# Optimization experiments

Measured on AMD Instinct MI355X. Metric: run time of the kernel, lower is better.

Reference implementation:

```python
import jax, jax.numpy as jnp
import numpy as np

H = 64  # hidden_size


def lstm_layer(x, Wih, Whh, bih, bhh):
    """Single LSTM layer, batch_first input x: [B, T, D]. Returns (hs [B,T,H], h_last [B,H]).
    PyTorch gate order: i, f, g, o."""
    B, T, _ = x.shape
    # Precompute input projections for all timesteps: [T, B, 4H]
    xg = jnp.einsum('btd,gd->tbg', x, Wih) + (bih + bhh)

    def step(carry, xt):
        h, c = carry
        gates = xt + h @ Whh.T  # [B, 4H]
        i, f, g, o = jnp.split(gates, 4, axis=-1)
        i = jax.nn.sigmoid(i)
        f = jax.nn.sigmoid(f)
        g = jnp.tanh(g)
        o = jax.nn.sigmoid(o)
        c = f * c + i * g
        h = o * jnp.tanh(c)
        return (h, c), h

    h0 = jnp.zeros((B, H), dtype=x.dtype)
    c0 = jnp.zeros((B, H), dtype=x.dtype)
    (h_last, _), hs = jax.lax.scan(step, (h0, c0), xg)
    return jnp.transpose(hs, (1, 0, 2)), h_last  # [B,T,H], [B,H]


def setup_inputs() -> dict:
    key = jax.random.key(0)
    ks = jax.random.split(key, 11)
    B, T, D = 1024, 512, 6
    s0 = 1.0 / np.sqrt(H)
    u = lambda k, shp: jax.random.uniform(k, shp, jnp.float32, -s0, s0)
    return {
        'x': jax.random.normal(ks[0], (B, T, D), jnp.float32),
        'Wih0': u(ks[1], (4 * H, D)),
        'Whh0': u(ks[2], (4 * H, H)),
        'bih0': u(ks[3], (4 * H,)),
        'bhh0': u(ks[4], (4 * H,)),
        'Wih1': u(ks[5], (4 * H, H)),
        'Whh1': u(ks[6], (4 * H, H)),
        'bih1': u(ks[7], (4 * H,)),
        'bhh1': u(ks[8], (4 * H,)),
        'W1': u(ks[9], (32, H)),
        'b1': jnp.zeros((32,), jnp.float32),
        'W2': u(ks[10], (1, 32)),
        'b2': jnp.zeros((1,), jnp.float32),
    }


def reference(x, Wih0, Whh0, bih0, bhh0, Wih1, Whh1, bih1, bhh1, W1, b1, W2, b2):
    # Layer 0 (dropout between layers is identity in eval mode)
    hs0, _ = lstm_layer(x, Wih0, Whh0, bih0, bhh0)
    # Layer 1: only last hidden state needed
    _, h_last = lstm_layer(hs0, Wih1, Whh1, bih1, bhh1)
    # MLP head: Linear -> ReLU -> (Dropout=identity) -> Linear -> Sigmoid
    z = jax.nn.relu(h_last @ W1.T + b1)
    out = jax.nn.sigmoid(z @ W2.T + b2)
    return out.squeeze()  # [B]
```

## Files before the change

kernel.cpp:

```cpp
#include <hip/hip_runtime.h>
#include <cstdint>

#define Hh 64
#define Tt 512
#define Dd 6
#define BB 4
#define NT 512
#define XS_STRIDE 3080
#define PREW 512

typedef short bf16x8 __attribute__((ext_vector_type(8)));
typedef float f32x4  __attribute__((ext_vector_type(4)));

#define MF(A, B, C) C = __builtin_amdgcn_mfma_f32_16x16x32_bf16(A, B, C, 0, 0, 0)

__device__ __forceinline__ float sigm(float v){
  return __builtin_amdgcn_rcpf(1.f + __expf(-v));
}
__device__ __forceinline__ float tanh_(float v){
  return 1.f - 2.f*__builtin_amdgcn_rcpf(1.f + __expf(2.f*v));
}
__device__ __forceinline__ unsigned short f2bf(float f){
  union { float f; unsigned u; } v; v.f = f;
  unsigned r = v.u + 0x7FFFu + ((v.u >> 16) & 1u);
  return (unsigned short)(r >> 16);
}
__device__ __forceinline__ float bf2f(unsigned short b){
  union { unsigned u; float f; } v; v.u = ((unsigned)b) << 16;
  return v.f;
}
__device__ __forceinline__ void split8(const float* w, bf16x8& hi, bf16x8& lo){
  #pragma unroll
  for (int i = 0; i < 8; ++i){
    unsigned short h_ = f2bf(w[i]);
    hi[i] = (short)h_;
    lo[i] = (short)f2bf(w[i] - bf2f(h_));
  }
}

__global__ __launch_bounds__(NT, 2)
void lstm2_mfma(const float* __restrict__ x,
                const float* __restrict__ Wih0, const float* __restrict__ Whh0,
                const float* __restrict__ bih0, const float* __restrict__ bhh0,
                const float* __restrict__ Wih1, const float* __restrict__ Whh1,
                const float* __restrict__ bih1, const float* __restrict__ bhh1,
                const float* __restrict__ W1, const float* __restrict__ b1,
                const float* __restrict__ W2, const float* __restrict__ b2,
                float* __restrict__ out)
{
  __shared__ __align__(16) float xs[BB*XS_STRIDE];
  __shared__ __align__(16) short hsb[2*2*1024];
  __shared__ __align__(16) float pre[8*PREW];
  __shared__ __align__(16) float h1f[BB*Hh];
  __shared__ float zs[BB*32];

  const int tid  = threadIdx.x;
  const int lane = tid & 63;
  const int wid  = tid >> 6;
  const int lr   = lane & 15;
  const int lg   = lane >> 4;
  const int l    = lane >> 5;
  const int jj   = (lane >> 2) & 7;
  const int bs   = lane & 3;
  const int jglob= wid*8 + jj;
  const int b0   = blockIdx.x * BB;

  #pragma unroll
  for (int bb = 0; bb < BB; ++bb){
    const float4* src = (const float4*)(x + (size_t)(b0+bb)*(Tt*Dd));
    float4* dst = (float4*)(xs + bb*XS_STRIDE);
    for (int i = tid; i < (Tt*Dd)/4; i += NT) dst[i] = src[i];
  }
  {
    int* hz = (int*)hsb;
    hz[tid] = 0; hz[tid+NT] = 0; hz[tid+2*NT] = 0; hz[tid+3*NT] = 0;
  }

  bf16x8 A0[2][2][2];
  bf16x8 A1[2][2][2][2];
  #pragma unroll
  for (int p = 0; p < 2; ++p){
    const int m = (lr&3)*64 + wid*8 + p*4 + (lr>>2);
    #pragma unroll
    for (int kt = 0; kt < 2; ++kt){
      const int off = m*64 + kt*32 + lg*8;
      float wbuf[8];
      *(float4*)&wbuf[0] = *(const float4*)&Whh0[off];
      *(float4*)&wbuf[4] = *(const float4*)&Whh0[off+4];
      split8(wbuf, A0[p][kt][0], A0[p][kt][1]);
      *(float4*)&wbuf[0] = *(const float4*)&Wih1[off];
      *(float4*)&wbuf[4] = *(const float4*)&Wih1[off+4];
      split8(wbuf, A1[p][0][kt][0], A1[p][0][kt][1]);
      *(float4*)&wbuf[0] = *(const float4*)&Whh1[off];
      *(float4*)&wbuf[4] = *(const float4*)&Whh1[off+4];
      split8(wbuf, A1[p][1][kt][0], A1[p][1][kt][1]);
    }
  }

  float bias_g[4], w0r[24];
  #pragma unroll
  for (int gt = 0; gt < 4; ++gt){
    const int row = gt*64 + jglob;
    if (l == 0){
      bias_g[gt] = bih0[row] + bhh0[row];
      #pragma unroll
      for (int d = 0; d < Dd; ++d) w0r[gt*6+d] = Wih0[row*Dd + d];
    } else {
      bias_g[gt] = bih1[row] + bhh1[row];
      #pragma unroll
      for (int d = 0; d < Dd; ++d) w0r[gt*6+d] = 0.f;
    }
  }

  const int boff0 = (lr*128 + lg*16)      ^ ((lr&7)<<4);
  const int boff1 = (lr*128 + 64 + lg*16) ^ ((lr&7)<<4);
  const int whi   = (bs*128     + jglob*2) ^ (bs<<4);
  const int wlo   = ((bs+4)*128 + jglob*2) ^ ((bs+4)<<4);
  float* preW = pre + wid*PREW;
  const int pwb  = lr*16 + ((lg ^ (lr&3)) << 2);
  const int lgp  = ((jj&3) ^ (bs&3)) << 2;
  const int sbase= (l*2 + (jj>>2))*128;
  const int prh  = sbase + bs*16 + lgp;
  const int prl  = sbase + (bs+4)*16 + lgp;

  float creg = 0.f;
  __syncthreads();

  if (l == 0){
    const float2* xv2 = (const float2*)(xs + bs*XS_STRIDE);
    float2 xa = xv2[0], xb = xv2[1], xc = xv2[2];
    float s[4];
    #pragma unroll
    for (int gt = 0; gt < 4; ++gt)
      s[gt] = bias_g[gt] + w0r[gt*6+0]*xa.x + w0r[gt*6+1]*xa.y
            + w0r[gt*6+2]*xb.x + w0r[gt*6+3]*xb.y
            + w0r[gt*6+4]*xc.x + w0r[gt*6+5]*xc.y;
    float iv = sigm(s[0]), fv = sigm(s[1]), gv = tanh_(s[2]), ov = sigm(s[3]);
    creg = fv*creg + iv*gv;
    float hval = ov * tanh_(creg);
    unsigned short hh = f2bf(hval);
    unsigned short hl = f2bf(hval - bf2f(hh));
    char* hw = (char*)hsb;
    *(short*)(hw + whi) = (short)hh;
    *(short*)(hw + wlo) = (short)hl;
  }
  __syncthreads();

  #pragma unroll 1
  for (int t = 0; t < Tt; ++t){
    const int buf = t & 1;
    const char* hb = (const char*)hsb + buf*4096;
    bf16x8 b00 = *(const bf16x8*)(hb + boff0);
    bf16x8 b01 = *(const bf16x8*)(hb + boff1);
    bf16x8 b10 = *(const bf16x8*)(hb + 2048 + boff0);
    bf16x8 b11 = *(const bf16x8*)(hb + 2048 + boff1);

    f32x4 a00 = {0,0,0,0}, a01 = {0,0,0,0}, a10 = {0,0,0,0}, a11 = {0,0,0,0};
    MF(A0[0][0][0], b00, a00); MF(A0[1][0][0], b00, a01);
    MF(A1[0][0][0][0], b00, a10); MF(A1[1][0][0][0], b00, a11);
    MF(A0[0][1][0], b01, a00); MF(A0[1][1][0], b01, a01);
    MF(A1[0][0][1][0], b01, a10); MF(A1[1][0][1][0], b01, a11);
    MF(A0[0][0][1], b00, a00); MF(A0[1][0][1], b00, a01);
    MF(A1[0][0][0][1], b00, a10); MF(A1[1][0][0][1], b00, a11);
    MF(A0[0][1][1], b01, a00); MF(A0[1][1][1], b01, a01);
    MF(A1[0][0][1][1], b01, a10); MF(A1[1][0][1][1], b01, a11);
    MF(A1[0][1][0][0], b10, a10); MF(A1[1][1][0][0], b10, a11);
    MF(A1[0][1][1][0], b11, a10); MF(A1[1][1][1][0], b11, a11);
    MF(A1[0][1][0][1], b10, a10); MF(A1[1][1][0][1], b10, a11);
    MF(A1[0][1][1][1], b11, a10); MF(A1[1][1][1][1], b11, a11);

    if (lr < 8){
      *(f32x4*)(preW + pwb)       = a00;
      *(f32x4*)(preW + pwb + 128) = a01;
      *(f32x4*)(preW + pwb + 256) = a10;
      *(f32x4*)(preW + pwb + 384) = a11;
    }

    if ((l == 1) | (t+1 < Tt)){
      f32x4 gh = *(const f32x4*)(preW + prh);
      f32x4 gl = *(const f32x4*)(preW + prl);
      float s0 = gh[0] + gl[0] + bias_g[0];
      float s1 = gh[1] + gl[1] + bias_g[1];
      float s2 = gh[2] + gl[2] + bias_g[2];
      float s3 = gh[3] + gl[3] + bias_g[3];
      if (l == 0){
        const float2* xv2 = (const float2*)(xs + bs*XS_STRIDE + (t+1)*Dd);
        float2 xa = xv2[0], xb = xv2[1], xc = xv2[2];
        s0 += w0r[ 0]*xa.x + w0r[ 1]*xa.y + w0r[ 2]*xb.x
            + w0r[ 3]*xb.y + w0r[ 4]*xc.x + w0r[ 5]*xc.y;
        s1 += w0r[ 6]*xa.x + w0r[ 7]*xa.y + w0r[ 8]*xb.x
            + w0r[ 9]*xb.y + w0r[10]*xc.x + w0r[11]*xc.y;
        s2 += w0r[12]*xa.x + w0r[13]*xa.y + w0r[14]*xb.x
            + w0r[15]*xb.y + w0r[16]*xc.x + w0r[17]*xc.y;
        s3 += w0r[18]*xa.x + w0r[19]*xa.y + w0r[20]*xb.x
            + w0r[21]*xb.y + w0r[22]*xc.x + w0r[23]*xc.y;
      }
      float iv = sigm(s0), fv = sigm(s1), gv = tanh_(s2), ov = sigm(s3);
      creg = fv*creg + iv*gv;
      float hval = ov * tanh_(creg);
      if ((l == 1) & (t == Tt-1)) h1f[bs*64 + jglob] = hval;
      unsigned short hh = f2bf(hval);
      unsigned short hl = f2bf(hval - bf2f(hh));
      char* hw = (char*)hsb + (buf^1)*4096 + l*2048;
      *(short*)(hw + whi) = (short)hh;
      *(short*)(hw + wlo) = (short)hl;
    }
    __syncthreads();
  }

  if (tid < BB*32){
    const int bsh = tid >> 5, m = tid & 31;
    float acc = b1[m];
    #pragma unroll
    for (int j = 0; j < Hh; ++j) acc += W1[m*Hh + j] * h1f[bsh*64 + j];
    zs[bsh*32 + m] = fmaxf(acc, 0.f);
  }
  __syncthreads();
  if (tid < BB){
    float acc = b2[0];
    #pragma unroll
    for (int m = 0; m < 32; ++m) acc += W2[m] * zs[tid*32 + m];
    out[b0 + tid] = sigm(acc);
  }
}

extern "C" void kernel_launch(void* const* d_in, const int* in_sizes, int n_in,
                              void* d_out, int out_size, void* d_ws, size_t ws_size,
                              hipStream_t stream) {
  const float* x    = (const float*)d_in[0];
  const float* Wih0 = (const float*)d_in[1];
  const float* Whh0 = (const float*)d_in[2];
  const float* bih0 = (const float*)d_in[3];
  const float* bhh0 = (const float*)d_in[4];
  const float* Wih1 = (const float*)d_in[5];
  const float* Whh1 = (const float*)d_in[6];
  const float* bih1 = (const float*)d_in[7];
  const float* bhh1 = (const float*)d_in[8];
  const float* W1   = (const float*)d_in[9];
  const float* b1   = (const float*)d_in[10];
  const float* W2   = (const float*)d_in[11];
  const float* b2   = (const float*)d_in[12];

  const int B = in_sizes[0] / (Tt*Dd);
  dim3 grid(B / BB), block(NT);
  hipLaunchKernelGGL(lstm2_mfma, grid, block, 0, stream,
                     x, Wih0, Whh0, bih0, bhh0, Wih1, Whh1, bih1, bhh1,
                     W1, b1, W2, b2, (float*)d_out);
}
```

Baseline: 458.6 us.

## Reduce MFMA gate outputs via lane shuffles and prefetch x from global

```diff
diff --git a/kernel.cpp b/kernel.cpp
--- a/kernel.cpp
+++ b/kernel.cpp
@@ -6,8 +6,6 @@
 #define Dd 6
 #define BB 4
 #define NT 512
-#define XS_STRIDE 3080
-#define PREW 512
 
 typedef short bf16x8 __attribute__((ext_vector_type(8)));
 typedef float f32x4  __attribute__((ext_vector_type(4)));
@@ -48,9 +46,7 @@
                 const float* __restrict__ W2, const float* __restrict__ b2,
                 float* __restrict__ out)
 {
-  __shared__ __align__(16) float xs[BB*XS_STRIDE];
   __shared__ __align__(16) short hsb[2*2*1024];
-  __shared__ __align__(16) float pre[8*PREW];
   __shared__ __align__(16) float h1f[BB*Hh];
   __shared__ float zs[BB*32];
 
@@ -59,18 +55,13 @@
   const int wid  = tid >> 6;
   const int lr   = lane & 15;
   const int lg   = lane >> 4;
-  const int l    = lane >> 5;
-  const int jj   = (lane >> 2) & 7;
-  const int bs   = lane & 3;
-  const int jglob= wid*8 + jj;
   const int b0   = blockIdx.x * BB;
 
-  #pragma unroll
-  for (int bb = 0; bb < BB; ++bb){
-    const float4* src = (const float4*)(x + (size_t)(b0+bb)*(Tt*Dd));
-    float4* dst = (float4*)(xs + bb*XS_STRIDE);
-    for (int i = tid; i < (Tt*Dd)/4; i += NT) dst[i] = src[i];
-  }
+  const int u_l  = lr >> 3;
+  const int u_p  = (lr >> 2) & 1;
+  const int u_bs = lr & 3;
+  const int u_j  = wid*8 + u_p*4 + lg;
+
   {
     int* hz = (int*)hsb;
     hz[tid] = 0; hz[tid+NT] = 0; hz[tid+2*NT] = 0; hz[tid+3*NT] = 0;
@@ -100,8 +91,8 @@
   float bias_g[4], w0r[24];
   #pragma unroll
   for (int gt = 0; gt < 4; ++gt){
-    const int row = gt*64 + jglob;
-    if (l == 0){
+    const int row = gt*64 + u_j;
+    if (u_l == 0){
       bias_g[gt] = bih0[row] + bhh0[row];
       #pragma unroll
       for (int d = 0; d < Dd; ++d) w0r[gt*6+d] = Wih0[row*Dd + d];
@@ -114,27 +105,24 @@
 
   const int boff0 = (lr*128 + lg*16)      ^ ((lr&7)<<4);
   const int boff1 = (lr*128 + 64 + lg*16) ^ ((lr&7)<<4);
-  const int whi   = (bs*128     + jglob*2) ^ (bs<<4);
-  const int wlo   = ((bs+4)*128 + jglob*2) ^ ((bs+4)<<4);
-  float* preW = pre + wid*PREW;
-  const int pwb  = lr*16 + ((lg ^ (lr&3)) << 2);
-  const int lgp  = ((jj&3) ^ (bs&3)) << 2;
-  const int sbase= (l*2 + (jj>>2))*128;
-  const int prh  = sbase + bs*16 + lgp;
-  const int prl  = sbase + (bs+4)*16 + lgp;
+  const int whi   = (u_bs*128     + u_j*2) ^ (u_bs<<4);
+  const int wlo   = ((u_bs+4)*128 + u_j*2) ^ ((u_bs+4)<<4);
+
+  const float2* px2 = (const float2*)(x + (size_t)(b0 + u_bs) * (Tt*Dd));
+  float2 xi0 = px2[0], xi1 = px2[1], xi2 = px2[2];
+  float2 xc0 = px2[3], xc1 = px2[4], xc2 = px2[5];
+  float2 xf0 = px2[6], xf1 = px2[7], xf2 = px2[8];
 
   float creg = 0.f;
   __syncthreads();
 
-  if (l == 0){
-    const float2* xv2 = (const float2*)(xs + bs*XS_STRIDE);
-    float2 xa = xv2[0], xb = xv2[1], xc = xv2[2];
+  if (u_l == 0){
     float s[4];
     #pragma unroll
     for (int gt = 0; gt < 4; ++gt)
-      s[gt] = bias_g[gt] + w0r[gt*6+0]*xa.x + w0r[gt*6+1]*xa.y
-            + w0r[gt*6+2]*xb.x + w0r[gt*6+3]*xb.y
-            + w0r[gt*6+4]*xc.x + w0r[gt*6+5]*xc.y;
+      s[gt] = bias_g[gt] + w0r[gt*6+0]*xi0.x + w0r[gt*6+1]*xi0.y
+            + w0r[gt*6+2]*xi1.x + w0r[gt*6+3]*xi1.y
+            + w0r[gt*6+4]*xi2.x + w0r[gt*6+5]*xi2.y;
     float iv = sigm(s[0]), fv = sigm(s[1]), gv = tanh_(s[2]), ov = sigm(s[3]);
     creg = fv*creg + iv*gv;
     float hval = ov * tanh_(creg);
@@ -146,8 +134,14 @@
   }
   __syncthreads();
 
-  #pragma unroll 1
+  #pragma unroll 2
   for (int t = 0; t < Tt; ++t){
+    float2 xn0, xn1, xn2;
+    {
+      const int tl = (t+3 < Tt) ? (t+3) : (Tt-1);
+      xn0 = px2[tl*3]; xn1 = px2[tl*3+1]; xn2 = px2[tl*3+2];
+    }
+
     const int buf = t & 1;
     const char* hb = (const char*)hsb + buf*4096;
     bf16x8 b00 = *(const bf16x8*)(hb + boff0);
@@ -157,54 +151,65 @@
 
     f32x4 a00 = {0,0,0,0}, a01 = {0,0,0,0}, a10 = {0,0,0,0}, a11 = {0,0,0,0};
     MF(A0[0][0][0], b00, a00); MF(A0[1][0][0], b00, a01);
+    MF(A0[0][1][0], b01, a00); MF(A0[1][1][0], b01, a01);
+    MF(A0[0][0][1], b00, a00); MF(A0[1][0][1], b00, a01);
+    MF(A0[0][1][1], b01, a00); MF(A0[1][1][1], b01, a01);
+
+    float g0[4];
+    #pragma unroll
+    for (int rg = 0; rg < 4; ++rg){
+      float own = (lr & 4) ? a01[rg] : a00[rg];
+      float snd = (lr & 4) ? a00[rg] : a01[rg];
+      g0[rg] = own + __shfl_xor(snd, 4);
+    }
+
     MF(A1[0][0][0][0], b00, a10); MF(A1[1][0][0][0], b00, a11);
-    MF(A0[0][1][0], b01, a00); MF(A0[1][1][0], b01, a01);
     MF(A1[0][0][1][0], b01, a10); MF(A1[1][0][1][0], b01, a11);
-    MF(A0[0][0][1], b00, a00); MF(A0[1][0][1], b00, a01);
     MF(A1[0][0][0][1], b00, a10); MF(A1[1][0][0][1], b00, a11);
-    MF(A0[0][1][1], b01, a00); MF(A0[1][1][1], b01, a01);
     MF(A1[0][0][1][1], b01, a10); MF(A1[1][0][1][1], b01, a11);
     MF(A1[0][1][0][0], b10, a10); MF(A1[1][1][0][0], b10, a11);
     MF(A1[0][1][1][0], b11, a10); MF(A1[1][1][1][0], b11, a11);
     MF(A1[0][1][0][1], b10, a10); MF(A1[1][1][0][1], b10, a11);
     MF(A1[0][1][1][1], b11, a10); MF(A1[1][1][1][1], b11, a11);
 
-    if (lr < 8){
-      *(f32x4*)(preW + pwb)       = a00;
-      *(f32x4*)(preW + pwb + 128) = a01;
-      *(f32x4*)(preW + pwb + 256) = a10;
-      *(f32x4*)(preW + pwb + 384) = a11;
-    }
-
-    if ((l == 1) | (t+1 < Tt)){
-      f32x4 gh = *(const f32x4*)(preW + prh);
-      f32x4 gl = *(const f32x4*)(preW + prl);
-      float s0 = gh[0] + gl[0] + bias_g[0];
-      float s1 = gh[1] + gl[1] + bias_g[1];
-      float s2 = gh[2] + gl[2] + bias_g[2];
-      float s3 = gh[3] + gl[3] + bias_g[3];
-      if (l == 0){
-        const float2* xv2 = (const float2*)(xs + bs*XS_STRIDE + (t+1)*Dd);
-        float2 xa = xv2[0], xb = xv2[1], xc = xv2[2];
-        s0 += w0r[ 0]*xa.x + w0r[ 1]*xa.y + w0r[ 2]*xb.x
-            + w0r[ 3]*xb.y + w0r[ 4]*xc.x + w0r[ 5]*xc.y;
-        s1 += w0r[ 6]*xa.x + w0r[ 7]*xa.y + w0r[ 8]*xb.x
-            + w0r[ 9]*xb.y + w0r[10]*xc.x + w0r[11]*xc.y;
-        s2 += w0r[12]*xa.x + w0r[13]*xa.y + w0r[14]*xb.x
-            + w0r[15]*xb.y + w0r[16]*xc.x + w0r[17]*xc.y;
-        s3 += w0r[18]*xa.x + w0r[19]*xa.y + w0r[20]*xb.x
-            + w0r[21]*xb.y + w0r[22]*xc.x + w0r[23]*xc.y;
+    float g1[4];
+    #pragma unroll
+    for (int rg = 0; rg < 4; ++rg){
+      float s10 = a10[rg] + __shfl_xor(a10[rg], 4);
+      float s11 = a11[rg] + __shfl_xor(a11[rg], 4);
+      float snd = (lr & 4) ? s11 : s10;
+      g1[rg] = __shfl_xor(snd, 8);
+    }
+
+    if ((u_l == 1) | (t+1 < Tt)){
+      float s0 = ((u_l == 0) ? g0[0] : g1[0]) + bias_g[0];
+      float s1 = ((u_l == 0) ? g0[1] : g1[1]) + bias_g[1];
+      float s2 = ((u_l == 0) ? g0[2] : g1[2]) + bias_g[2];
+      float s3 = ((u_l == 0) ? g0[3] : g1[3]) + bias_g[3];
+      if (u_l == 0){
+        s0 += w0r[ 0]*xc0.x + w0r[ 1]*xc0.y + w0r[ 2]*xc1.x
+            + w0r[ 3]*xc1.y + w0r[ 4]*xc2.x + w0r[ 5]*xc2.y;
+        s1 += w0r[ 6]*xc0.x + w0r[ 7]*xc0.y + w0r[ 8]*xc1.x
+            + w0r[ 9]*xc1.y + w0r[10]*xc2.x + w0r[11]*xc2.y;
+        s2 += w0r[12]*xc0.x + w0r[13]*xc0.y + w0r[14]*xc1.x
+            + w0r[15]*xc1.y + w0r[16]*xc2.x + w0r[17]*xc2.y;
+        s3 += w0r[18]*xc0.x + w0r[19]*xc0.y + w0r[20]*xc1.x
+            + w0r[21]*xc1.y + w0r[22]*xc2.x + w0r[23]*xc2.y;
       }
       float iv = sigm(s0), fv = sigm(s1), gv = tanh_(s2), ov = sigm(s3);
       creg = fv*creg + iv*gv;
       float hval = ov * tanh_(creg);
-      if ((l == 1) & (t == Tt-1)) h1f[bs*64 + jglob] = hval;
+      if ((u_l == 1) & (t == Tt-1)) h1f[u_bs*64 + u_j] = hval;
       unsigned short hh = f2bf(hval);
       unsigned short hl = f2bf(hval - bf2f(hh));
-      char* hw = (char*)hsb + (buf^1)*4096 + l*2048;
+      char* hw = (char*)hsb + (buf^1)*4096 + u_l*2048;
       *(short*)(hw + whi) = (short)hh;
       *(short*)(hw + wlo) = (short)hl;
     }
+
+    xc0 = xf0; xc1 = xf1; xc2 = xf2;
+    xf0 = xn0; xf1 = xn1; xf2 = xn2;
+
     __syncthreads();
   }
 
```

Result: faster. 436.0 us (-4.9%).

## Split layers into producer/consumer warp groups synchronized by LDS flag counters

Applied to the files above, without the earlier changes.

```diff
diff --git a/kernel.cpp b/kernel.cpp
--- a/kernel.cpp
+++ b/kernel.cpp
@@ -6,13 +6,11 @@
 #define Dd 6
 #define BB 4
 #define NT 512
-#define XS_STRIDE 3080
-#define PREW 512
 
 typedef short bf16x8 __attribute__((ext_vector_type(8)));
 typedef float f32x4  __attribute__((ext_vector_type(4)));
 
-#define MF(A, B, C) C = __builtin_amdgcn_mfma_f32_16x16x32_bf16(A, B, C, 0, 0, 0)
+#define MF(A,B,C) C = __builtin_amdgcn_mfma_f32_16x16x32_bf16(A,B,C,0,0,0)
 
 __device__ __forceinline__ float sigm(float v){
   return __builtin_amdgcn_rcpf(1.f + __expf(-v));
@@ -37,176 +35,239 @@
     lo[i] = (short)f2bf(w[i] - bf2f(h_));
   }
 }
-
-__global__ __launch_bounds__(NT, 2)
-void lstm2_mfma(const float* __restrict__ x,
-                const float* __restrict__ Wih0, const float* __restrict__ Whh0,
-                const float* __restrict__ bih0, const float* __restrict__ bhh0,
-                const float* __restrict__ Wih1, const float* __restrict__ Whh1,
-                const float* __restrict__ bih1, const float* __restrict__ bhh1,
-                const float* __restrict__ W1, const float* __restrict__ b1,
-                const float* __restrict__ W2, const float* __restrict__ b2,
-                float* __restrict__ out)
+__device__ __forceinline__ void splitH(float v, unsigned short& hh, unsigned short& hl){
+  union { float f; unsigned u; } a; a.f = v;
+  hh = (unsigned short)(a.u >> 16);
+  float r = v - bf2f(hh);
+  union { float f; unsigned u; } b; b.f = r;
+  hl = (unsigned short)(b.u >> 16);
+}
+__device__ __forceinline__ void spinGE(int* f, int target){
+  while (__hip_atomic_load(f, __ATOMIC_ACQUIRE, __HIP_MEMORY_SCOPE_WORKGROUP) < target)
+    __builtin_amdgcn_s_sleep(1);
+}
+__device__ __forceinline__ void incFlag(int* f, int lane){
+  asm volatile("s_waitcnt lgkmcnt(0)" ::: "memory");
+  if (lane == 0)
+    __hip_atomic_fetch_add(f, 1, __ATOMIC_RELEASE, __HIP_MEMORY_SCOPE_WORKGROUP);
+}
+
+__global__ __launch_bounds__(NT, 1)
+void lstm2_ps(const float* __restrict__ x,
+              const float* __restrict__ Wih0, const float* __restrict__ Whh0,
+              const float* __restrict__ bih0, const float* __restrict__ bhh0,
+              const float* __restrict__ Wih1, const float* __restrict__ Whh1,
+              const float* __restrict__ bih1, const float* __restrict__ bhh1,
+              const float* __restrict__ W1, const float* __restrict__ b1,
+              const float* __restrict__ W2, const float* __restrict__ b2,
+              float* __restrict__ out)
 {
-  __shared__ __align__(16) float xs[BB*XS_STRIDE];
-  __shared__ __align__(16) short hsb[2*2*1024];
-  __shared__ __align__(16) float pre[8*PREW];
+  __shared__ __align__(16) short h0ring[4*1024];
+  __shared__ __align__(16) short h1buf [2*1024];
+  __shared__ __align__(16) f32x4 stage[8*128];
   __shared__ __align__(16) float h1f[BB*Hh];
   __shared__ float zs[BB*32];
+  __shared__ int flags[2];
 
   const int tid  = threadIdx.x;
   const int lane = tid & 63;
   const int wid  = tid >> 6;
   const int lr   = lane & 15;
   const int lg   = lane >> 4;
-  const int l    = lane >> 5;
-  const int jj   = (lane >> 2) & 7;
-  const int bs   = lane & 3;
-  const int jglob= wid*8 + jj;
+  const int eng  = wid >> 2;
+  const int w4   = wid & 3;
   const int b0   = blockIdx.x * BB;
 
-  #pragma unroll
-  for (int bb = 0; bb < BB; ++bb){
-    const float4* src = (const float4*)(x + (size_t)(b0+bb)*(Tt*Dd));
-    float4* dst = (float4*)(xs + bb*XS_STRIDE);
-    for (int i = tid; i < (Tt*Dd)/4; i += NT) dst[i] = src[i];
-  }
+  const int c_p  = lane >> 4;
+  const int c_j  = (lane >> 2) & 3;
+  const int c_bs = lane & 3;
+  const int u_j  = w4*16 + c_p*4 + c_j;
+
   {
-    int* hz = (int*)hsb;
-    hz[tid] = 0; hz[tid+NT] = 0; hz[tid+2*NT] = 0; hz[tid+3*NT] = 0;
-  }
-
-  bf16x8 A0[2][2][2];
-  bf16x8 A1[2][2][2][2];
-  #pragma unroll
-  for (int p = 0; p < 2; ++p){
-    const int m = (lr&3)*64 + wid*8 + p*4 + (lr>>2);
-    #pragma unroll
-    for (int kt = 0; kt < 2; ++kt){
-      const int off = m*64 + kt*32 + lg*8;
-      float wbuf[8];
-      *(float4*)&wbuf[0] = *(const float4*)&Whh0[off];
-      *(float4*)&wbuf[4] = *(const float4*)&Whh0[off+4];
-      split8(wbuf, A0[p][kt][0], A0[p][kt][1]);
-      *(float4*)&wbuf[0] = *(const float4*)&Wih1[off];
-      *(float4*)&wbuf[4] = *(const float4*)&Wih1[off+4];
-      split8(wbuf, A1[p][0][kt][0], A1[p][0][kt][1]);
-      *(float4*)&wbuf[0] = *(const float4*)&Whh1[off];
-      *(float4*)&wbuf[4] = *(const float4*)&Whh1[off+4];
-      split8(wbuf, A1[p][1][kt][0], A1[p][1][kt][1]);
-    }
-  }
-
-  float bias_g[4], w0r[24];
-  #pragma unroll
-  for (int gt = 0; gt < 4; ++gt){
-    const int row = gt*64 + jglob;
-    if (l == 0){
-      bias_g[gt] = bih0[row] + bhh0[row];
-      #pragma unroll
-      for (int d = 0; d < Dd; ++d) w0r[gt*6+d] = Wih0[row*Dd + d];
-    } else {
-      bias_g[gt] = bih1[row] + bhh1[row];
-      #pragma unroll
-      for (int d = 0; d < Dd; ++d) w0r[gt*6+d] = 0.f;
-    }
-  }
+    int* hz = (int*)h0ring;
+    #pragma unroll
+    for (int i = 0; i < 4; ++i) hz[tid + i*NT] = 0;
+    int* h1z = (int*)h1buf;
+    h1z[tid] = 0; h1z[tid + NT] = 0;
+  }
+  if (tid == 0){ flags[0] = 0; flags[1] = 0; }
 
   const int boff0 = (lr*128 + lg*16)      ^ ((lr&7)<<4);
   const int boff1 = (lr*128 + 64 + lg*16) ^ ((lr&7)<<4);
-  const int whi   = (bs*128     + jglob*2) ^ (bs<<4);
-  const int wlo   = ((bs+4)*128 + jglob*2) ^ ((bs+4)<<4);
-  float* preW = pre + wid*PREW;
-  const int pwb  = lr*16 + ((lg ^ (lr&3)) << 2);
-  const int lgp  = ((jj&3) ^ (bs&3)) << 2;
-  const int sbase= (l*2 + (jj>>2))*128;
-  const int prh  = sbase + bs*16 + lgp;
-  const int prl  = sbase + (bs+4)*16 + lgp;
-
-  float creg = 0.f;
+  const int whi   = (c_bs*128     + u_j*2) ^ (c_bs<<4);
+  const int wlo   = ((c_bs+4)*128 + u_j*2) ^ ((c_bs+4)<<4);
+  const int stW   = wid*128 + ((lr>>2)&1)*64 + lg*4 + (lr&3);
+  const int stR   = wid*128 + lane;
+
   __syncthreads();
 
-  if (l == 0){
-    const float2* xv2 = (const float2*)(xs + bs*XS_STRIDE);
-    float2 xa = xv2[0], xb = xv2[1], xc = xv2[2];
-    float s[4];
-    #pragma unroll
-    for (int gt = 0; gt < 4; ++gt)
-      s[gt] = bias_g[gt] + w0r[gt*6+0]*xa.x + w0r[gt*6+1]*xa.y
-            + w0r[gt*6+2]*xb.x + w0r[gt*6+3]*xb.y
-            + w0r[gt*6+4]*xc.x + w0r[gt*6+5]*xc.y;
-    float iv = sigm(s[0]), fv = sigm(s[1]), gv = tanh_(s[2]), ov = sigm(s[3]);
-    creg = fv*creg + iv*gv;
-    float hval = ov * tanh_(creg);
-    unsigned short hh = f2bf(hval);
-    unsigned short hl = f2bf(hval - bf2f(hh));
-    char* hw = (char*)hsb;
-    *(short*)(hw + whi) = (short)hh;
-    *(short*)(hw + wlo) = (short)hl;
-  }
-  __syncthreads();
-
-  #pragma unroll 1
-  for (int t = 0; t < Tt; ++t){
-    const int buf = t & 1;
-    const char* hb = (const char*)hsb + buf*4096;
-    bf16x8 b00 = *(const bf16x8*)(hb + boff0);
-    bf16x8 b01 = *(const bf16x8*)(hb + boff1);
-    bf16x8 b10 = *(const bf16x8*)(hb + 2048 + boff0);
-    bf16x8 b11 = *(const bf16x8*)(hb + 2048 + boff1);
-
-    f32x4 a00 = {0,0,0,0}, a01 = {0,0,0,0}, a10 = {0,0,0,0}, a11 = {0,0,0,0};
-    MF(A0[0][0][0], b00, a00); MF(A0[1][0][0], b00, a01);
-    MF(A1[0][0][0][0], b00, a10); MF(A1[1][0][0][0], b00, a11);
-    MF(A0[0][1][0], b01, a00); MF(A0[1][1][0], b01, a01);
-    MF(A1[0][0][1][0], b01, a10); MF(A1[1][0][1][0], b01, a11);
-    MF(A0[0][0][1], b00, a00); MF(A0[1][0][1], b00, a01);
-    MF(A1[0][0][0][1], b00, a10); MF(A1[1][0][0][1], b00, a11);
-    MF(A0[0][1][1], b01, a00); MF(A0[1][1][1], b01, a01);
-    MF(A1[0][0][1][1], b01, a10); MF(A1[1][0][1][1], b01, a11);
-    MF(A1[0][1][0][0], b10, a10); MF(A1[1][1][0][0], b10, a11);
-    MF(A1[0][1][1][0], b11, a10); MF(A1[1][1][1][0], b11, a11);
-    MF(A1[0][1][0][1], b10, a10); MF(A1[1][1][0][1], b10, a11);
-    MF(A1[0][1][1][1], b11, a10); MF(A1[1][1][1][1], b11, a11);
-
-    if (lr < 8){
-      *(f32x4*)(preW + pwb)       = a00;
-      *(f32x4*)(preW + pwb + 128) = a01;
-      *(f32x4*)(preW + pwb + 256) = a10;
-      *(f32x4*)(preW + pwb + 384) = a11;
-    }
-
-    if ((l == 1) | (t+1 < Tt)){
-      f32x4 gh = *(const f32x4*)(preW + prh);
-      f32x4 gl = *(const f32x4*)(preW + prl);
+  if (eng == 0){
+    bf16x8 A0[4][2][2];
+    #pragma unroll
+    for (int p = 0; p < 4; ++p){
+      const int m = (lr&3)*64 + w4*16 + p*4 + (lr>>2);
+      #pragma unroll
+      for (int kt = 0; kt < 2; ++kt){
+        const int off = m*64 + kt*32 + lg*8;
+        float wbuf[8];
+        *(float4*)&wbuf[0] = *(const float4*)&Whh0[off];
+        *(float4*)&wbuf[4] = *(const float4*)&Whh0[off+4];
+        split8(wbuf, A0[p][kt][0], A0[p][kt][1]);
+      }
+    }
+    float bias_g[4], w0r[24];
+    #pragma unroll
+    for (int gt = 0; gt < 4; ++gt){
+      const int row = gt*64 + u_j;
+      bias_g[gt] = bih0[row] + bhh0[row];
+      #pragma unroll
+      for (int d = 0; d < Dd; ++d) w0r[gt*6+d] = Wih0[row*Dd + d];
+    }
+    const float2* px2 = (const float2*)(x + (size_t)(b0 + c_bs) * (Tt*Dd));
+    float creg = 0.f;
+
+    {
+      float2 xa = px2[0], xb = px2[1], xc = px2[2];
+      float s[4];
+      #pragma unroll
+      for (int gt = 0; gt < 4; ++gt)
+        s[gt] = bias_g[gt] + w0r[gt*6+0]*xa.x + w0r[gt*6+1]*xa.y
+              + w0r[gt*6+2]*xb.x + w0r[gt*6+3]*xb.y
+              + w0r[gt*6+4]*xc.x + w0r[gt*6+5]*xc.y;
+      float iv = sigm(s[0]), fv = sigm(s[1]), gv = tanh_(s[2]), ov = sigm(s[3]);
+      creg = fv*creg + iv*gv;
+      float hval = ov * tanh_(creg);
+      unsigned short hh, hl; splitH(hval, hh, hl);
+      char* hw = (char*)h0ring;
+      *(short*)(hw + whi) = (short)hh;
+      *(short*)(hw + wlo) = (short)hl;
+      incFlag(&flags[0], lane);
+    }
+
+    #pragma unroll 1
+    for (int t = 1; t < Tt; ++t){
+      spinGE(&flags[0], 4*t);
+      const char* hb = (const char*)h0ring + ((t-1)&3)*2048;
+      bf16x8 b00 = *(const bf16x8*)(hb + boff0);
+      bf16x8 b01 = *(const bf16x8*)(hb + boff1);
+      float2 x0 = px2[t*3], x1 = px2[t*3+1], x2 = px2[t*3+2];
+
+      f32x4 a[4];
+      #pragma unroll
+      for (int p = 0; p < 4; ++p) a[p] = (f32x4){0,0,0,0};
+      #pragma unroll
+      for (int p = 0; p < 4; ++p) MF(A0[p][0][0], b00, a[p]);
+      #pragma unroll
+      for (int p = 0; p < 4; ++p) MF(A0[p][1][0], b01, a[p]);
+      #pragma unroll
+      for (int p = 0; p < 4; ++p) MF(A0[p][0][1], b00, a[p]);
+      #pragma unroll
+      for (int p = 0; p < 4; ++p) MF(A0[p][1][1], b01, a[p]);
+
+      if (lr < 8){
+        stage[stW     ] = a[0];
+        stage[stW + 16] = a[1];
+        stage[stW + 32] = a[2];
+        stage[stW + 48] = a[3];
+      }
+      f32x4 gh = stage[stR];
+      f32x4 gl = stage[stR + 64];
+      float s0 = gh[0] + gl[0] + bias_g[0]
+               + w0r[ 0]*x0.x + w0r[ 1]*x0.y + w0r[ 2]*x1.x
+               + w0r[ 3]*x1.y + w0r[ 4]*x2.x + w0r[ 5]*x2.y;
+      float s1 = gh[1] + gl[1] + bias_g[1]
+               + w0r[ 6]*x0.x + w0r[ 7]*x0.y + w0r[ 8]*x1.x
+               + w0r[ 9]*x1.y + w0r[10]*x2.x + w0r[11]*x2.y;
+      float s2 = gh[2] + gl[2] + bias_g[2]
+               + w0r[12]*x0.x + w0r[13]*x0.y + w0r[14]*x1.x
+               + w0r[15]*x1.y + w0r[16]*x2.x + w0r[17]*x2.y;
+      float s3 = gh[3] + gl[3] + bias_g[3]
+               + w0r[18]*x0.x + w0r[19]*x0.y + w0r[20]*x1.x
+               + w0r[21]*x1.y + w0r[22]*x2.x + w0r[23]*x2.y;
+      float iv = sigm(s0), fv = sigm(s1), gv = tanh_(s2), ov = sigm(s3);
+      creg = fv*creg + iv*gv;
+      float hval = ov * tanh_(creg);
+      unsigned short hh, hl; splitH(hval, hh, hl);
+
+      if (t >= 4) spinGE(&flags[1], 4*(t-3));
+      char* hw = (char*)h0ring + (t&3)*2048;
+      *(short*)(hw + whi) = (short)hh;
+      *(short*)(hw + wlo) = (short)hl;
+      incFlag(&flags[0], lane);
+    }
+  } else {
+    bf16x8 A1i[4][2][2], A1h[4][2][2];
+    #pragma unroll
+    for (int p = 0; p < 4; ++p){
+      const int m = (lr&3)*64 + w4*16 + p*4 + (lr>>2);
+      #pragma unroll
+      for (int kt = 0; kt < 2; ++kt){
+        const int off = m*64 + kt*32 + lg*8;
+        float wbuf[8];
+        *(float4*)&wbuf[0] = *(const float4*)&Wih1[off];
+        *(float4*)&wbuf[4] = *(const float4*)&Wih1[off+4];
+        split8(wbuf, A1i[p][kt][0], A1i[p][kt][1]);
+        *(float4*)&wbuf[0] = *(const float4*)&Whh1[off];
+        *(float4*)&wbuf[4] = *(const float4*)&Whh1[off+4];
+        split8(wbuf, A1h[p][kt][0], A1h[p][kt][1]);
+      }
+    }
+    float bias_g[4];
+    #pragma unroll
+    for (int gt = 0; gt < 4; ++gt){
+      const int row = gt*64 + u_j;
+      bias_g[gt] = bih1[row] + bhh1[row];
+    }
+    float creg = 0.f;
+
+    #pragma unroll 1
+    for (int t = 0; t < Tt; ++t){
+      spinGE(&flags[0], 4*(t+1));
+      spinGE(&flags[1], 4*t);
+      const char* hb0 = (const char*)h0ring + (t&3)*2048;
+      const char* hb1 = (const char*)h1buf + ((t&1)^1)*2048;
+      bf16x8 b00 = *(const bf16x8*)(hb0 + boff0);
+      bf16x8 b01 = *(const bf16x8*)(hb0 + boff1);
+      bf16x8 b10 = *(const bf16x8*)(hb1 + boff0);
+      bf16x8 b11 = *(const bf16x8*)(hb1 + boff1);
+
+      f32x4 ai[4], ah[4];
+      #pragma unroll
+      for (int p = 0; p < 4; ++p){ ai[p] = (f32x4){0,0,0,0}; ah[p] = (f32x4){0,0,0,0}; }
+      #pragma unroll
+      for (int p = 0; p < 4; ++p){ MF(A1i[p][0][0], b00, ai[p]); MF(A1h[p][0][0], b10, ah[p]); }
+      #pragma unroll
+      for (int p = 0; p < 4; ++p){ MF(A1i[p][1][0], b01, ai[p]); MF(A1h[p][1][0], b11, ah[p]); }
+      #pragma unroll
+      for (int p = 0; p < 4; ++p){ MF(A1i[p][0][1], b00, ai[p]); MF(A1h[p][0][1], b10, ah[p]); }
+      #pragma unroll
+      for (int p = 0; p < 4; ++p){ MF(A1i[p][1][1], b01, ai[p]); MF(A1h[p][1][1], b11, ah[p]); }
+
+      if (lr < 8){
+        stage[stW     ] = ai[0] + ah[0];
+        stage[stW + 16] = ai[1] + ah[1];
+        stage[stW + 32] = ai[2] + ah[2];
+        stage[stW + 48] = ai[3] + ah[3];
+      }
+      f32x4 gh = stage[stR];
+      f32x4 gl = stage[stR + 64];
       float s0 = gh[0] + gl[0] + bias_g[0];
       float s1 = gh[1] + gl[1] + bias_g[1];
       float s2 = gh[2] + gl[2] + bias_g[2];
       float s3 = gh[3] + gl[3] + bias_g[3];
-      if (l == 0){
-        const float2* xv2 = (const float2*)(xs + bs*XS_STRIDE + (t+1)*Dd);
-        float2 xa = xv2[0], xb = xv2[1], xc = xv2[2];
-        s0 += w0r[ 0]*xa.x + w0r[ 1]*xa.y + w0r[ 2]*xb.x
-            + w0r[ 3]*xb.y + w0r[ 4]*xc.x + w0r[ 5]*xc.y;
-        s1 += w0r[ 6]*xa.x + w0r[ 7]*xa.y + w0r[ 8]*xb.x
-            + w0r[ 9]*xb.y + w0r[10]*xc.x + w0r[11]*xc.y;
-        s2 += w0r[12]*xa.x + w0r[13]*xa.y + w0r[14]*xb.x
-            + w0r[15]*xb.y + w0r[16]*xc.x + w0r[17]*xc.y;
-        s3 += w0r[18]*xa.x + w0r[19]*xa.y + w0r[20]*xb.x
-            + w0r[21]*xb.y + w0r[22]*xc.x + w0r[23]*xc.y;
-      }
       float iv = sigm(s0), fv = sigm(s1), gv = tanh_(s2), ov = sigm(s3);
       creg = fv*creg + iv*gv;
       float hval = ov * tanh_(creg);
-      if ((l == 1) & (t == Tt-1)) h1f[bs*64 + jglob] = hval;
-      unsigned short hh = f2bf(hval);
-      unsigned short hl = f2bf(hval - bf2f(hh));
-      char* hw = (char*)hsb + (buf^1)*4096 + l*2048;
+      if (t == Tt-1) h1f[c_bs*64 + u_j] = hval;
+      unsigned short hh, hl; splitH(hval, hh, hl);
+      char* hw = (char*)h1buf + (t&1)*2048;
       *(short*)(hw + whi) = (short)hh;
       *(short*)(hw + wlo) = (short)hl;
-    }
-    __syncthreads();
-  }
+      incFlag(&flags[1], lane);
+    }
+  }
+
+  __syncthreads();
 
   if (tid < BB*32){
     const int bsh = tid >> 5, m = tid & 31;
@@ -243,7 +304,7 @@
 
   const int B = in_sizes[0] / (Tt*Dd);
   dim3 grid(B / BB), block(NT);
-  hipLaunchKernelGGL(lstm2_mfma, grid, block, 0, stream,
+  hipLaunchKernelGGL(lstm2_ps, grid, block, 0, stream,
                      x, Wih0, Whh0, bih0, bhh0, Wih1, Whh1, bih1, bhh1,
                      W1, b1, W2, b2, (float*)d_out);
 }
```

Result: faster. 430.6 us (-6.1%).
